# Performance work log

Measured on AMD Instinct MI355X. Metric: run time of the kernel, lower is better.

The kernel has to match this reference:

```python
import jax, jax.numpy as jnp
import numpy as np
from jax import lax

PAD_IDX = 9182


def setup_inputs() -> dict:
    key = jax.random.key(0)
    ks = jax.random.split(key, 16)
    B, S = 16, 256
    V, E, H, SH = 32000, 512, 1024, 1024
    sc = 0.05
    embed = jax.random.normal(ks[0], (V, E), jnp.float32) * sc
    embed = embed.at[PAD_IDX].set(0.0)  # padding_idx row
    inp = {
        "context_encoding": jax.random.normal(ks[1], (B, 1, SH), jnp.float32),
        "target": jax.random.randint(ks[2], (B, S), 0, V),
        "embed": embed,                                              # embed_in.weight (shared out proj)
        "W_s2d": jax.random.normal(ks[3], (H, SH), jnp.float32) * sc,   # ses_to_dec
        "b_s2d": jax.random.normal(ks[4], (H,), jnp.float32) * sc,
        "W_dec_inf": jax.random.normal(ks[5], (2 * E, H), jnp.float32) * sc,
        "W_ses_inf": jax.random.normal(ks[6], (2 * E, SH), jnp.float32) * sc,
        "W_emb_inf": jax.random.normal(ks[7], (2 * E, E), jnp.float32) * sc,
        "b_emb_inf": jax.random.normal(ks[8], (2 * E,), jnp.float32) * sc,
        "W_ih": jax.random.normal(ks[9], (3 * H, E), jnp.float32) * sc,  # GRU input weights
        "W_hh": jax.random.normal(ks[10], (3 * H, H), jnp.float32) * sc,  # GRU hidden weights
        "b_ih": jax.random.normal(ks[11], (3 * H,), jnp.float32) * sc,
        "b_hh": jax.random.normal(ks[12], (3 * H,), jnp.float32) * sc,
    }
    return inp


def _decode(context_encoding, embed, W_s2d, b_s2d, W_dec_inf, W_ses_inf,
            W_emb_inf, b_emb_inf, W_ih, W_hh, b_ih, b_hh, target):
    B, S = target.shape
    ctx = context_encoding[:, 0]                    # [B, SH]
    ses_inf = ctx @ W_ses_inf.T                     # [B, 2E]
    h0 = jnp.tanh(ctx @ W_s2d.T + b_s2d)            # [B, H] init decoder hidden

    emb = embed[target]                             # [B, S, E]
    emb_inf = emb @ W_emb_inf.T + b_emb_inf         # [B, S, 2E]
    x_proj = emb @ W_ih.T + b_ih                    # [B, S, 3H] precomputed GRU input gates

    def gru_step(h, xp):
        gh = h @ W_hh.T + b_hh                      # [B, 3H]
        xr, xz, xn = jnp.split(xp, 3, axis=-1)
        hr, hz, hn = jnp.split(gh, 3, axis=-1)
        r = jax.nn.sigmoid(xr + hr)
        z = jax.nn.sigmoid(xz + hz)
        n = jnp.tanh(xn + r * hn)
        h_new = (1.0 - z) * n + z * h
        return h_new, h_new

    _, hs = lax.scan(gru_step, h0, jnp.swapaxes(x_proj, 0, 1))  # [S, B, H]
    hs = jnp.swapaxes(hs, 0, 1)                     # [B, S, H]

    total = hs @ W_dec_inf.T + ses_inf[:, None, :] + emb_inf  # [B, S, 2E]
    mx = total.reshape(B, S, -1, 2).max(axis=-1)    # maxout pairs -> [B, S, E]
    logits = mx @ embed.T                           # shared embedding out proj [B, S, V]
    return logits


def reference(context_encoding, target, embed, W_s2d, b_s2d, W_dec_inf,
              W_ses_inf, W_emb_inf, b_emb_inf, W_ih, W_hh, b_ih, b_hh):
    dec_o = _decode(context_encoding, embed, W_s2d, b_s2d, W_dec_inf,
                    W_ses_inf, W_emb_inf, b_emb_inf, W_ih, W_hh, b_ih, b_hh,
                    target)
    return dec_o
```

## Files before the change

### kernel.cpp

```cpp
#include <hip/hip_runtime.h>

typedef unsigned short u16;
typedef unsigned int u32;
typedef __attribute__((ext_vector_type(8))) __bf16 bf16x8;
typedef __attribute__((ext_vector_type(4))) float f32x4;
typedef __attribute__((ext_vector_type(4))) u32 u32x4;

#define ASYNC16(g, l) __builtin_amdgcn_global_load_lds( \
    (const __attribute__((address_space(1))) unsigned int*)(g), \
    (__attribute__((address_space(3))) unsigned int*)(l), 16, 0, 0)

__device__ __forceinline__ u16 f2bf(float f){
  unsigned u = __float_as_uint(f);
  unsigned r = u + 0x7fffu + ((u >> 16) & 1u);
  return (u16)(r >> 16);
}

__global__ __launch_bounds__(256) void f2bf_kernel(const float* __restrict__ in,
                                                   u16* __restrict__ out, int n){
  int i = (blockIdx.x * 256 + threadIdx.x) * 8;
  if (i >= n) return;
  float4 a = *(const float4*)&in[i];
  float4 b = *(const float4*)&in[i + 4];
  u16 r[8] = {f2bf(a.x), f2bf(a.y), f2bf(a.z), f2bf(a.w),
              f2bf(b.x), f2bf(b.y), f2bf(b.z), f2bf(b.w)};
  *(uint4*)&out[i] = *(const uint4*)r;
}

__global__ __launch_bounds__(256) void ctx_kernel(const float* __restrict__ ctx,
    const float* __restrict__ Wses, const float* __restrict__ Ws2d,
    const float* __restrict__ bs2d, float* __restrict__ sesinf,
    float* __restrict__ h0f, u16* __restrict__ h0bf){
  int id = blockIdx.x * 4 + (threadIdx.x >> 6);
  int lane = threadIdx.x & 63;
  int n = id & 1023, b = (id >> 10) & 15, mat = id >> 14;
  const float* w = (mat ? Ws2d : Wses) + (size_t)n * 1024;
  const float* x = ctx + (size_t)b * 1024;
  float v = 0.f;
  #pragma unroll 4
  for (int k = lane; k < 1024; k += 64) v += x[k] * w[k];
  #pragma unroll
  for (int off = 32; off; off >>= 1) v += __shfl_down(v, off);
  if (lane == 0){
    if (mat == 0) sesinf[b * 1024 + n] = v;
    else {
      float t = tanhf(v + bs2d[n]);
      h0f[b * 1024 + n] = t;
      h0bf[b * 1024 + n] = f2bf(t);
    }
  }
}

__global__ void gather_kernel(const int* __restrict__ target,
                              const u16* __restrict__ embedBF, u16* __restrict__ embBF){
  int i = blockIdx.x;
  int t = target[i];
  int lane = threadIdx.x;
  *(uint4*)&embBF[(size_t)i * 512 + lane * 8] =
      *(const uint4*)&embedBF[(size_t)t * 512 + lane * 8];
}

__global__ __launch_bounds__(256) void maxout_kernel(const float* __restrict__ total,
                                                     u16* __restrict__ mx){
  int idx = blockIdx.x * 256 + threadIdx.x;
  int r = idx >> 9, e = idx & 511;
  float a = total[(size_t)r * 1024 + 2 * e];
  float b = total[(size_t)r * 1024 + 2 * e + 1];
  mx[idx] = f2bf(fmaxf(a, b));
}

template<int EPI, int SWZ>
__global__ __launch_bounds__(256) void gemm_bt(
    const u16* __restrict__ A, const u16* __restrict__ B, float* __restrict__ C,
    int M, int N, int K,
    const float* __restrict__ bias, const float* __restrict__ add0,
    const float* __restrict__ add1)
{
  __shared__ u16 sA[2][128 * 32];
  __shared__ u16 sB[2][128 * 32];
  int bx = blockIdx.x, by = blockIdx.y;
  if (SWZ){
    int nwg = gridDim.x * gridDim.y;
    int wg = by * gridDim.x + bx;
    int q = nwg >> 3;
    int nw = (wg & 7) * q + (wg >> 3);
    bx = nw % gridDim.x; by = nw / gridDim.x;
  }
  const int n0 = bx * 128;
  const int m0 = by * 128;
  const int tid = threadIdx.x;
  const int lane = tid & 63;
  const int wid = tid >> 6;
  const int wm = (wid >> 1) * 64, wn = (wid & 1) * 64;
  const int l15 = lane & 15, kg = (lane >> 4) * 8;
  (void)M;

  f32x4 zero = {0.f, 0.f, 0.f, 0.f};
  f32x4 acc[4][4];
  #pragma unroll
  for (int m = 0; m < 4; m++)
    #pragma unroll
    for (int n = 0; n < 4; n++) acc[m][n] = zero;

  auto stage = [&](int buf, int kk){
    const u16* Ab = A + (size_t)m0 * K + kk;
    const u16* Bb = B + (size_t)n0 * K + kk;
    #pragma unroll
    for (int j = 0; j < 2; j++){
      int c = j * 256 + tid;
      ASYNC16(Ab + (size_t)(c >> 2) * K + (c & 3) * 8, &sA[buf][c * 8]);
    }
    #pragma unroll
    for (int j = 0; j < 2; j++){
      int c = j * 256 + tid;
      ASYNC16(Bb + (size_t)(c >> 2) * K + (c & 3) * 8, &sB[buf][c * 8]);
    }
  };

  stage(0, 0);
  int cur = 0;
  for (int kk = 0; kk < K; kk += 32){
    __syncthreads();
    if (kk + 32 < K) stage(cur ^ 1, kk + 32);
    bf16x8 af[4], bf_[4];
    #pragma unroll
    for (int m = 0; m < 4; m++)
      af[m] = *(const bf16x8*)&sA[cur][(wm + m * 16 + l15) * 32 + kg];
    #pragma unroll
    for (int n = 0; n < 4; n++)
      bf_[n] = *(const bf16x8*)&sB[cur][(wn + n * 16 + l15) * 32 + kg];
    #pragma unroll
    for (int m = 0; m < 4; m++)
      #pragma unroll
      for (int n = 0; n < 4; n++)
        acc[m][n] = __builtin_amdgcn_mfma_f32_16x16x32_bf16(af[m], bf_[n], acc[m][n], 0, 0, 0);
    cur ^= 1;
  }

  const int rb = m0 + wm + (lane >> 4) * 4;
  const int cb = n0 + wn + l15;
  #pragma unroll
  for (int m = 0; m < 4; m++){
    #pragma unroll
    for (int n = 0; n < 4; n++){
      #pragma unroll
      for (int i = 0; i < 4; i++){
        int row = rb + m * 16 + i;
        int col = cb + n * 16;
        float v = acc[m][n][i];
        if (EPI == 1) v += bias[col];
        if (EPI == 2) v += add0[(row >> 8) * N + col] + add1[(size_t)row * N + col];
        C[(size_t)row * N + col] = v;
      }
    }
  }
}

#define GRU_NWG 64
#define GRU_LDS 136192

__global__ __launch_bounds__(256) void gru_kernel(
    const u16* __restrict__ WhhBF, const float* __restrict__ bhh,
    const float* __restrict__ xproj, const float* __restrict__ h0f,
    const u16* __restrict__ h0bf, u16* __restrict__ hsBF, int* flags)
{
  extern __shared__ char smem[];
  u16*  Wl   = (u16*)smem;
  u16*  hb   = Wl + 48 * 1032;
  float* gbuf = (float*)(smem + 132096);
  float* hown = gbuf + 3 * 256;

  const int g = blockIdx.x;
  const int j0 = g * 16;
  const int tid = threadIdx.x;
  const int lane = tid & 63;
  const int wid = tid >> 6;
  const int bb = tid >> 4, jj = tid & 15;

  for (int c = tid; c < 48 * 128; c += 256){
    int r = c >> 7, cg = (c & 127) * 8;
    int gate = r >> 4, n = r & 15;
    *(uint4*)&Wl[r * 1032 + cg] =
        *(const uint4*)&WhhBF[(size_t)(gate * 1024 + j0 + n) * 1024 + cg];
  }
  hown[bb * 16 + jj] = h0f[bb * 1024 + j0 + jj];
  const float bh0 = bhh[j0 + jj];
  const float bh1 = bhh[1024 + j0 + jj];
  const float bh2 = bhh[2048 + j0 + jj];
  u32* hs32 = (u32*)hsBF;
  __syncthreads();

  for (int s = 0; s < 256; ++s){
    if (s == 0){
      #pragma unroll
      for (int k = 0; k < 8; k++){
        int c = tid + k * 256;
        int b = c >> 7, cg = (c & 127) * 8;
        *(uint4*)&hb[b * 1032 + cg] = *(const uint4*)&h0bf[b * 1024 + cg];
      }
    } else {
      u32x4 r[8];
      #pragma unroll
      for (int k = 0; k < 8; k++){
        int c = tid + k * 256;
        int b = c >> 7, cg = (c & 127) * 8;
        const u16* src = &hsBF[(size_t)((b << 8) + s - 1) * 1024 + cg];
        asm volatile("global_load_dwordx4 %0, %1, off sc1"
                     : "=v"(r[k]) : "v"(src) : "memory");
      }
      asm volatile("s_waitcnt vmcnt(0)" ::: "memory");
      #pragma unroll
      for (int k = 0; k < 8; k++){
        int c = tid + k * 256;
        int b = c >> 7, cg = (c & 127) * 8;
        *(u32x4*)&hb[b * 1032 + cg] = r[k];
      }
    }

    const float* xp = xproj + ((size_t)(bb << 8) + s) * 3072;
    float xr = xp[j0 + jj], xz = xp[1024 + j0 + jj], xn = xp[2048 + j0 + jj];
    __syncthreads();

    if (wid < 3){
      f32x4 acc0 = {0.f, 0.f, 0.f, 0.f};
      f32x4 acc1 = {0.f, 0.f, 0.f, 0.f};
      const int l15 = lane & 15, kg = (lane >> 4) * 8;
      const u16* wrow = &Wl[(wid * 16 + l15) * 1032];
      const u16* hrow = &hb[l15 * 1032];
      #pragma unroll 8
      for (int kk = 0; kk < 1024; kk += 64){
        bf16x8 a0 = *(const bf16x8*)&hrow[kk + kg];
        bf16x8 w0 = *(const bf16x8*)&wrow[kk + kg];
        acc0 = __builtin_amdgcn_mfma_f32_16x16x32_bf16(a0, w0, acc0, 0, 0, 0);
        bf16x8 a1 = *(const bf16x8*)&hrow[kk + 32 + kg];
        bf16x8 w1 = *(const bf16x8*)&wrow[kk + 32 + kg];
        acc1 = __builtin_amdgcn_mfma_f32_16x16x32_bf16(a1, w1, acc1, 0, 0, 0);
      }
      #pragma unroll
      for (int i = 0; i < 4; ++i)
        gbuf[wid * 256 + ((lane >> 4) * 4 + i) * 16 + l15] = acc0[i] + acc1[i];
    }
    __syncthreads();

    {
      float hr = gbuf[0 * 256 + bb * 16 + jj] + bh0;
      float hz = gbuf[1 * 256 + bb * 16 + jj] + bh1;
      float hn = gbuf[2 * 256 + bb * 16 + jj] + bh2;
      float r = 1.f / (1.f + __expf(-(xr + hr)));
      float z = 1.f / (1.f + __expf(-(xz + hz)));
      float nn = tanhf(xn + r * hn);
      float hnew = (1.f - z) * nn + z * hown[bb * 16 + jj];
      hown[bb * 16 + jj] = hnew;
      float hnext = __shfl_down(hnew, 1);
      if ((jj & 1) == 0){
        u32 pack = (u32)f2bf(hnew) | ((u32)f2bf(hnext) << 16);
        size_t e = (size_t)((bb << 8) + s) * 1024 + j0 + jj;
        __hip_atomic_store(&hs32[e >> 1], pack, __ATOMIC_RELAXED,
                           __HIP_MEMORY_SCOPE_AGENT);
      }
    }

    if (s < 255){
      asm volatile("s_waitcnt vmcnt(0)" ::: "memory");
      __syncthreads();
      if (tid == 0)
        __hip_atomic_store(&flags[g * 32], s + 1, __ATOMIC_RELAXED,
                           __HIP_MEMORY_SCOPE_AGENT);
      if (wid == 0){
        while (__hip_atomic_load(&flags[lane * 32], __ATOMIC_RELAXED,
                                 __HIP_MEMORY_SCOPE_AGENT) <= s)
          __builtin_amdgcn_s_sleep(1);
      }
      __syncthreads();
    }
  }
}

extern "C" void kernel_launch(void* const* d_in, const int* in_sizes, int n_in,
                              void* d_out, int out_size, void* d_ws, size_t ws_size,
                              hipStream_t stream)
{
  const float* ctx    = (const float*)d_in[0];
  const int*   target = (const int*)d_in[1];
  const float* embed  = (const float*)d_in[2];
  const float* Ws2d   = (const float*)d_in[3];
  const float* bs2d   = (const float*)d_in[4];
  const float* Wdec   = (const float*)d_in[5];
  const float* Wses   = (const float*)d_in[6];
  const float* Wemb   = (const float*)d_in[7];
  const float* bemb   = (const float*)d_in[8];
  const float* Wih    = (const float*)d_in[9];
  const float* Whh    = (const float*)d_in[10];
  const float* bih    = (const float*)d_in[11];
  const float* bhh    = (const float*)d_in[12];
  float* out = (float*)d_out;

  char* ws = (char*)d_ws;
  size_t off = 0;
  auto alloc = [&](size_t bytes)->char*{
    char* p = ws + off; off += (bytes + 255) & ~(size_t)255; return p;
  };
  u16*   embedBF = (u16*)alloc(32000ull * 512 * 2);
  u16*   WihBF   = (u16*)alloc(3072ull * 512 * 2);
  u16*   WembBF  = (u16*)alloc(1024ull * 512 * 2);
  u16*   WdecBF  = (u16*)alloc(1024ull * 1024 * 2);
  u16*   WhhBF   = (u16*)alloc(3072ull * 1024 * 2);
  u16*   embBF   = (u16*)alloc(4096ull * 512 * 2);
  float* xproj   = (float*)alloc(4096ull * 3072 * 4);
  float* embinf  = (float*)alloc(4096ull * 1024 * 4);
  float* sesinf  = (float*)alloc(16ull * 1024 * 4);
  float* h0f     = (float*)alloc(16ull * 1024 * 4);
  u16*   h0bf    = (u16*)alloc(16ull * 1024 * 2);
  u16*   hsBF    = (u16*)alloc(4096ull * 1024 * 2);
  float* total   = (float*)alloc(4096ull * 1024 * 4);
  u16*   mxBF    = (u16*)alloc(4096ull * 512 * 2);
  int*   flags   = (int*)alloc(16384);
  (void)ws_size; (void)in_sizes; (void)n_in; (void)out_size;

  hipFuncSetAttribute((const void*)gru_kernel,
                      hipFuncAttributeMaxDynamicSharedMemorySize, GRU_LDS);
  hipMemsetAsync(flags, 0, 16384, stream);

  auto conv = [&](const float* in, u16* o, size_t n){
    f2bf_kernel<<<dim3((unsigned)((n / 8 + 255) / 256)), 256, 0, stream>>>(in, o, (int)n);
  };
  conv(embed, embedBF, 32000ull * 512);
  conv(Wih,   WihBF,   3072ull * 512);
  conv(Wemb,  WembBF,  1024ull * 512);
  conv(Wdec,  WdecBF,  1024ull * 1024);
  conv(Whh,   WhhBF,   3072ull * 1024);

  ctx_kernel<<<8192, 256, 0, stream>>>(ctx, Wses, Ws2d, bs2d, sesinf, h0f, h0bf);
  gather_kernel<<<4096, 64, 0, stream>>>(target, embedBF, embBF);

  gemm_bt<1,0><<<dim3(3072 / 128, 4096 / 128), 256, 0, stream>>>(
      embBF, WihBF, xproj, 4096, 3072, 512, bih, nullptr, nullptr);
  gemm_bt<1,0><<<dim3(1024 / 128, 4096 / 128), 256, 0, stream>>>(
      embBF, WembBF, embinf, 4096, 1024, 512, bemb, nullptr, nullptr);

  gru_kernel<<<GRU_NWG, 256, GRU_LDS, stream>>>(WhhBF, bhh, xproj, h0f, h0bf, hsBF, flags);

  gemm_bt<2,0><<<dim3(1024 / 128, 4096 / 128), 256, 0, stream>>>(
      hsBF, WdecBF, total, 4096, 1024, 1024, nullptr, sesinf, embinf);
  maxout_kernel<<<8192, 256, 0, stream>>>(total, mxBF);

  gemm_bt<0,1><<<dim3(32000 / 128, 4096 / 128), 256, 0, stream>>>(
      mxBF, embedBF, out, 4096, 32000, 512, nullptr, nullptr, nullptr);
}
```

Measured before the change: 1.332 ms.

## Replace GRU flag barrier with step-tagged double-buffered hidden-state exchange

The per-step global flag barrier across the 64 GRU workgroups is removed. Each hidden value is now published together with its step number in a double-buffered exchange buffer, and consumers poll until every word carries the expected tag. This drops the wait-for-stores, the extra block syncs and the serialized flag spin, and it issues the xproj loads before the exchange wait. The cost is more polling traffic and a reliance on relaxed-atomic visibility with parity-based buffer reuse.

```diff
diff --git a/kernel.cpp b/kernel.cpp
--- a/kernel.cpp
+++ b/kernel.cpp
@@ -162,7 +162,7 @@
 __global__ __launch_bounds__(256) void gru_kernel(
     const u16* __restrict__ WhhBF, const float* __restrict__ bhh,
     const float* __restrict__ xproj, const float* __restrict__ h0f,
-    const u16* __restrict__ h0bf, u16* __restrict__ hsBF, int* flags)
+    const u16* __restrict__ h0bf, u16* __restrict__ hsBF, u32* __restrict__ xb)
 {
   extern __shared__ char smem[];
   u16*  Wl   = (u16*)smem;
@@ -187,10 +187,12 @@
   const float bh0 = bhh[j0 + jj];
   const float bh1 = bhh[1024 + j0 + jj];
   const float bh2 = bhh[2048 + j0 + jj];
-  u32* hs32 = (u32*)hsBF;
   __syncthreads();
 
   for (int s = 0; s < 256; ++s){
+    const float* xp = xproj + ((size_t)(bb << 8) + s) * 3072;
+    float xr = xp[j0 + jj], xz = xp[1024 + j0 + jj], xn = xp[2048 + j0 + jj];
+
     if (s == 0){
       #pragma unroll
       for (int k = 0; k < 8; k++){
@@ -199,26 +201,34 @@
         *(uint4*)&hb[b * 1032 + cg] = *(const uint4*)&h0bf[b * 1024 + cg];
       }
     } else {
-      u32x4 r[8];
-      #pragma unroll
-      for (int k = 0; k < 8; k++){
-        int c = tid + k * 256;
-        int b = c >> 7, cg = (c & 127) * 8;
-        const u16* src = &hsBF[(size_t)((b << 8) + s - 1) * 1024 + cg];
-        asm volatile("global_load_dwordx4 %0, %1, off sc1"
-                     : "=v"(r[k]) : "v"(src) : "memory");
-      }
-      asm volatile("s_waitcnt vmcnt(0)" ::: "memory");
-      #pragma unroll
-      for (int k = 0; k < 8; k++){
-        int c = tid + k * 256;
-        int b = c >> 7, cg = (c & 127) * 8;
-        *(u32x4*)&hb[b * 1032 + cg] = r[k];
-      }
-    }
-
-    const float* xp = xproj + ((size_t)(bb << 8) + s) * 3072;
-    float xr = xp[j0 + jj], xz = xp[1024 + j0 + jj], xn = xp[2048 + j0 + jj];
+      const u32* base = xb + ((u32)(s & 1) << 14) + tid * 4;
+      u32 need = 0xFFFFu;
+      u32x4 v[16];
+      while (need){
+        #pragma unroll
+        for (int k = 0; k < 16; k++){
+          if (need & (1u << k)){
+            asm volatile("global_load_dwordx4 %0, %1, off sc1"
+                         : "=v"(v[k]) : "v"(base + k * 1024) : "memory");
+          }
+        }
+        asm volatile("s_waitcnt vmcnt(0)" ::: "memory");
+        #pragma unroll
+        for (int k = 0; k < 16; k++){
+          if (need & (1u << k)){
+            u32 m = ((v[k][0] ^ (u32)s) | (v[k][1] ^ (u32)s) |
+                     (v[k][2] ^ (u32)s) | (v[k][3] ^ (u32)s)) & 0xFFFFu;
+            if (m == 0){
+              u32 dd[2];
+              dd[0] = (v[k][0] >> 16) | (v[k][1] & 0xFFFF0000u);
+              dd[1] = (v[k][2] >> 16) | (v[k][3] & 0xFFFF0000u);
+              *(uint2*)&hb[k * 1032 + tid * 4] = *(const uint2*)dd;
+              need &= ~(1u << k);
+            }
+          }
+        }
+      }
+    }
     __syncthreads();
 
     if (wid < 3){
@@ -251,27 +261,13 @@
       float nn = tanhf(xn + r * hn);
       float hnew = (1.f - z) * nn + z * hown[bb * 16 + jj];
       hown[bb * 16 + jj] = hnew;
-      float hnext = __shfl_down(hnew, 1);
-      if ((jj & 1) == 0){
-        u32 pack = (u32)f2bf(hnew) | ((u32)f2bf(hnext) << 16);
-        size_t e = (size_t)((bb << 8) + s) * 1024 + j0 + jj;
-        __hip_atomic_store(&hs32[e >> 1], pack, __ATOMIC_RELAXED,
-                           __HIP_MEMORY_SCOPE_AGENT);
-      }
-    }
-
-    if (s < 255){
-      asm volatile("s_waitcnt vmcnt(0)" ::: "memory");
-      __syncthreads();
-      if (tid == 0)
-        __hip_atomic_store(&flags[g * 32], s + 1, __ATOMIC_RELAXED,
-                           __HIP_MEMORY_SCOPE_AGENT);
-      if (wid == 0){
-        while (__hip_atomic_load(&flags[lane * 32], __ATOMIC_RELAXED,
-                                 __HIP_MEMORY_SCOPE_AGENT) <= s)
-          __builtin_amdgcn_s_sleep(1);
-      }
-      __syncthreads();
+      u16 hv = f2bf(hnew);
+      hsBF[((size_t)(bb << 8) + s) * 1024 + j0 + jj] = hv;
+      if (s < 255){
+        u32 pack = ((u32)hv << 16) | (u32)(s + 1);
+        __hip_atomic_store(&xb[((u32)((s + 1) & 1) << 14) + bb * 1024 + j0 + jj],
+                           pack, __ATOMIC_RELAXED, __HIP_MEMORY_SCOPE_AGENT);
+      }
     }
   }
 }
@@ -314,12 +310,12 @@
   u16*   hsBF    = (u16*)alloc(4096ull * 1024 * 2);
   float* total   = (float*)alloc(4096ull * 1024 * 4);
   u16*   mxBF    = (u16*)alloc(4096ull * 512 * 2);
-  int*   flags   = (int*)alloc(16384);
+  u32*   xbuf    = (u32*)alloc(2ull * 16 * 1024 * 4);
   (void)ws_size; (void)in_sizes; (void)n_in; (void)out_size;
 
   hipFuncSetAttribute((const void*)gru_kernel,
                       hipFuncAttributeMaxDynamicSharedMemorySize, GRU_LDS);
-  hipMemsetAsync(flags, 0, 16384, stream);
+  hipMemsetAsync(xbuf, 0, 2ull * 16 * 1024 * 4, stream);
 
   auto conv = [&](const float* in, u16* o, size_t n){
     f2bf_kernel<<<dim3((unsigned)((n / 8 + 255) / 256)), 256, 0, stream>>>(in, o, (int)n);
@@ -338,7 +334,7 @@
   gemm_bt<1,0><<<dim3(1024 / 128, 4096 / 128), 256, 0, stream>>>(
       embBF, WembBF, embinf, 4096, 1024, 512, bemb, nullptr, nullptr);
 
-  gru_kernel<<<GRU_NWG, 256, GRU_LDS, stream>>>(WhhBF, bhh, xproj, h0f, h0bf, hsBF, flags);
+  gru_kernel<<<GRU_NWG, 256, GRU_LDS, stream>>>(WhhBF, bhh, xproj, h0f, h0bf, hsBF, xbuf);
 
   gemm_bt<2,0><<<dim3(1024 / 128, 4096 / 128), 256, 0, stream>>>(
       hsBF, WdecBF, total, 4096, 1024, 1024, nullptr, sesinf, embinf);
```

Result: slower. 1.640 ms (+23.1%).
